# Performance work log

Measured on AMD Instinct MI355X. Metric: run time of the kernel, lower is better.

Reference implementation:

```python
import jax, jax.numpy as jnp
import numpy as np

SIZE = 5
DIM = 64


def setup_inputs() -> dict:
    key = jax.random.key(0)
    k0, k1, k2, k3, k4 = jax.random.split(key, 5)
    bs, C, H, W = 4, 3, 1024, 1024
    x = jax.random.uniform(k0, (bs, C, H, W), dtype=jnp.float32)
    n_off = SIZE * SIZE
    # conv1x1_{i}_E: Conv2d(1, DIM, 1) -> weight (DIM,1,1,1) ~= vector (DIM,), bias (DIM,)
    # conv1x1_{i}_S: Conv2d(DIM, 1, 1) -> weight (1,DIM,1,1) ~= vector (DIM,), bias ()
    wE = jax.random.normal(k1, (n_off, DIM), dtype=jnp.float32)            # fan_in=1 -> U(-1,1)-ish scale
    bE = jax.random.normal(k2, (n_off, DIM), dtype=jnp.float32) * 0.5
    wS = jax.random.normal(k3, (n_off, DIM), dtype=jnp.float32) * (1.0 / np.sqrt(DIM))
    bS = jax.random.normal(k4, (n_off,), dtype=jnp.float32) * 0.1
    return {"x": x, "wE": wE, "bE": bE, "wS": wS, "bS": bS}


def reference(x, wE, bE, wS, bS):
    size = SIZE
    pad = size // 2
    bs, C, H, W = x.shape
    xc = jnp.clip(x, 0.0, 1.0).reshape(bs * C, H, W)            # (N,H,W)
    xp = jnp.pad(xc, ((0, 0), (pad, pad), (pad, pad)), mode="reflect")
    # 25 shifted views, stacked: (K, N, H, W). Small fixed python loop over offsets.
    shifts = jnp.stack([xp[:, i:i + H, j:j + W]
                        for i in range(size) for j in range(size)])
    # Per offset k, S(E(x)) is linear in x (no nonlinearity between the 1x1 convs):
    #   out_k = (wS_k . wE_k) * x_k + (wS_k . bE_k + bS_k)
    a = jnp.einsum("kd,kd->k", wS, wE)                          # per-offset scale
    c = jnp.einsum("kd,kd->k", wS, bE) + bS                     # per-offset pixel-constant bias
    out = jnp.einsum("k,knhw->nhw", a, shifts) + c.sum()
    out = out / (size * size)
    out = jnp.clip(out, 0.0, 1.0)
    return out.reshape(bs, C, H, W)
```

## Files before the change

kernel.cpp:

```cpp
#include <hip/hip_runtime.h>
#include <hip/hip_bf16.h>


#define HH 1024
#define WW 1024
#define NIMG 12
#define TBH 8
#define ROWS (TBH + 4)
#define PF 6

typedef float f32x4 __attribute__((ext_vector_type(4)));
typedef float f32x2 __attribute__((ext_vector_type(2)));

__device__ __forceinline__ float readlane_f(float v, int lane) {
    return __int_as_float(__builtin_amdgcn_readlane(__float_as_int(v), lane));
}

__device__ __forceinline__ float sgpr_bcast(float v) {
    return __int_as_float(__builtin_amdgcn_readfirstlane(__float_as_int(v)));
}

__device__ __forceinline__ float dot4(f32x4 a, f32x4 b) {
    return a.x * b.x + a.y * b.y + a.z * b.z + a.w * b.w;
}

__device__ __forceinline__ f32x4 clip01v4(f32x4 v) {
    f32x4 z = {0.f, 0.f, 0.f, 0.f};
    f32x4 o = {1.f, 1.f, 1.f, 1.f};
    return __builtin_elementwise_min(__builtin_elementwise_max(v, z), o);
}

__device__ __forceinline__ f32x2 clip01v2(f32x2 v) {
    f32x2 z = {0.f, 0.f};
    f32x2 o = {1.f, 1.f};
    return __builtin_elementwise_min(__builtin_elementwise_max(v, z), o);
}

__global__ __launch_bounds__(256) void conv5_kernel(const float* __restrict__ x,
                                                    const float* __restrict__ wE,
                                                    const float* __restrict__ bE,
                                                    const float* __restrict__ wS,
                                                    const float* __restrict__ bS,
                                                    float* __restrict__ out) {
    int lane = threadIdx.x & 63;

    float apass[2], cacc = 0.f;
    #pragma unroll
    for (int p = 0; p < 2; ++p) {
        int k = p * 16 + (lane >> 2);
        float a = 0.f;
        if (k < 25) {
            int base = k * 64 + (lane & 3) * 16;
            #pragma unroll
            for (int i = 0; i < 4; ++i) {
                f32x4 sv = *(const f32x4*)(wS + base + 4 * i);
                f32x4 ev = *(const f32x4*)(wE + base + 4 * i);
                f32x4 bv = *(const f32x4*)(bE + base + 4 * i);
                a += dot4(sv, ev);
                cacc += dot4(sv, bv);
            }
        }
        a += __shfl_xor(a, 1);
        a += __shfl_xor(a, 2);
        apass[p] = a;
    }
    if (lane < 25) cacc += bS[lane];
    #pragma unroll
    for (int off = 32; off; off >>= 1) cacc += __shfl_xor(cacc, off);
    float bias = sgpr_bcast(cacc * (1.f / 25.f));
    f32x2 bias2 = {bias, bias};

    float wv[25];
    #pragma unroll
    for (int k = 0; k < 16; ++k) wv[k] = readlane_f(apass[0], 4 * k) * (1.f / 25.f);
    #pragma unroll
    for (int k = 16; k < 25; ++k) wv[k] = readlane_f(apass[1], 4 * (k - 16)) * (1.f / 25.f);

    int nwg = gridDim.x;
    int cpx = nwg >> 3;
    int l = (blockIdx.x & 7) * cpx + (blockIdx.x >> 3);
    int img = l >> 7;
    int rb = l & 127;
    int row0 = rb * TBH;

    const float* src = x + (size_t)img * (HH * WW);
    int tid = threadIdx.x;
    int cbase = tid * 4;

    bool lt = (cbase == 0);
    bool rt = (cbase == 1020);
    int qa = lt ? 0 : cbase - 2;
    int qb = rt ? 1020 : cbase + 2;

    auto rowptr = [&](int ir) -> const float* {
        int prow = row0 - 2 + ir;
        int sr = prow < 0 ? -prow : (prow >= HH ? 2 * HH - 2 - prow : prow);
        return src + (size_t)sr * WW;
    };

    f32x4 bufA[PF], bufB[PF];
    f32x2 acc[5][2];

    #pragma unroll
    for (int ir = 0; ir < PF; ++ir) {
        const float* rp = rowptr(ir);
        bufA[ir] = *(const f32x4*)(rp + qa);
        bufB[ir] = *(const f32x4*)(rp + qb);
    }
    __builtin_amdgcn_sched_barrier(0);

    float* op = out + (size_t)img * (HH * WW) + (size_t)row0 * WW + cbase;

    #pragma unroll
    for (int ir = 0; ir < ROWS; ++ir) {
        f32x4 A = bufA[ir % PF];
        f32x4 B = bufB[ir % PF];
        if (ir + PF < ROWS) {
            const float* rp = rowptr(ir + PF);
            bufA[ir % PF] = *(const f32x4*)(rp + qa);
            bufB[ir % PF] = *(const f32x4*)(rp + qb);
        }

        A = clip01v4(A);
        B = clip01v4(B);

        float r8[8] = {A.x, A.y, A.z, A.w, B.x, B.y, B.z, B.w};
        r8[0] = lt ? A.z : r8[0];
        r8[2] = lt ? A.x : r8[2];
        r8[3] = lt ? A.y : r8[3];
        r8[4] = rt ? B.z : r8[4];
        r8[5] = rt ? B.w : r8[5];
        r8[7] = rt ? B.y : r8[7];

        f32x2 pr[7];
        #pragma unroll
        for (int j = 0; j < 7; ++j) { pr[j].x = r8[j]; pr[j].y = r8[j + 1]; }

        if (ir < TBH) {
            acc[ir % 5][0] = bias2;
            acc[ir % 5][1] = bias2;
        }

        #pragma unroll
        for (int dr = 0; dr < 5; ++dr) {
            int orow = ir - dr;
            if (orow < 0 || orow >= TBH) continue;
            #pragma unroll
            for (int j = 0; j < 5; ++j) {
                float wj = wv[dr * 5 + j];
                f32x2 w2 = {wj, wj};
                acc[orow % 5][0] += pr[j] * w2;
                acc[orow % 5][1] += pr[j + 2] * w2;
            }
        }

        if (ir >= 4) {
            int orow = ir - 4;
            f32x2 lo = clip01v2(acc[orow % 5][0]);
            f32x2 hi = clip01v2(acc[orow % 5][1]);
            f32x4 o = {lo.x, lo.y, hi.x, hi.y};
            *(f32x4*)(op + (size_t)orow * WW) = o;
        }
    }
}

extern "C" void kernel_launch(void* const* d_in, const int* in_sizes, int n_in,
                              void* d_out, int out_size, void* d_ws, size_t ws_size,
                              hipStream_t stream) {
    const float* x  = (const float*)d_in[0];
    const float* wE = (const float*)d_in[1];
    const float* bE = (const float*)d_in[2];
    const float* wS = (const float*)d_in[3];
    const float* bS = (const float*)d_in[4];
    float* out = (float*)d_out;

    int nblocks = NIMG * (HH / TBH);
    conv5_kernel<<<nblocks, 256, 0, stream>>>(x, wE, bE, wS, bS, out);
}
```

Before: 25.67 us.

## Switch to persistent grid computing one output row per iteration

Replaces the 8-row register-blocked sliding window with a fixed grid of 2048 blocks, each looping over 6 single output rows strided across the whole tensor. Every output row now reloads its 5 input rows directly, so there is no vertical reuse in registers and each row is fetched about 5x instead of about 1.5x. The intent is to cut register pressure and per-block tail effects and to spread work evenly, relying on L2/MALL to absorb the redundant row loads. The risk is extra cache traffic and less in-flight prefetch depth.

```diff
diff --git a/kernel.cpp b/kernel.cpp
--- a/kernel.cpp
+++ b/kernel.cpp
@@ -5,9 +5,8 @@
 #define HH 1024
 #define WW 1024
 #define NIMG 12
-#define TBH 8
-#define ROWS (TBH + 4)
-#define PF 6
+#define NB 2048
+#define ITERS 6
 
 typedef float f32x4 __attribute__((ext_vector_type(4)));
 typedef float f32x2 __attribute__((ext_vector_type(2)));
@@ -15,21 +14,17 @@
 __device__ __forceinline__ float readlane_f(float v, int lane) {
     return __int_as_float(__builtin_amdgcn_readlane(__float_as_int(v), lane));
 }
-
 __device__ __forceinline__ float sgpr_bcast(float v) {
     return __int_as_float(__builtin_amdgcn_readfirstlane(__float_as_int(v)));
 }
-
 __device__ __forceinline__ float dot4(f32x4 a, f32x4 b) {
     return a.x * b.x + a.y * b.y + a.z * b.z + a.w * b.w;
 }
-
 __device__ __forceinline__ f32x4 clip01v4(f32x4 v) {
     f32x4 z = {0.f, 0.f, 0.f, 0.f};
     f32x4 o = {1.f, 1.f, 1.f, 1.f};
     return __builtin_elementwise_min(__builtin_elementwise_max(v, z), o);
 }
-
 __device__ __forceinline__ f32x2 clip01v2(f32x2 v) {
     f32x2 z = {0.f, 0.f};
     f32x2 o = {1.f, 1.f};
@@ -42,7 +37,8 @@
                                                     const float* __restrict__ wS,
                                                     const float* __restrict__ bS,
                                                     float* __restrict__ out) {
-    int lane = threadIdx.x & 63;
+    int tid  = threadIdx.x;
+    int lane = tid & 63;
 
     float apass[2], cacc = 0.f;
     #pragma unroll
@@ -76,91 +72,62 @@
     #pragma unroll
     for (int k = 16; k < 25; ++k) wv[k] = readlane_f(apass[1], 4 * (k - 16)) * (1.f / 25.f);
 
-    int nwg = gridDim.x;
-    int cpx = nwg >> 3;
-    int l = (blockIdx.x & 7) * cpx + (blockIdx.x >> 3);
-    int img = l >> 7;
-    int rb = l & 127;
-    int row0 = rb * TBH;
+    int l = (blockIdx.x & 7) * (NB >> 3) + (blockIdx.x >> 3);
 
-    const float* src = x + (size_t)img * (HH * WW);
-    int tid = threadIdx.x;
     int cbase = tid * 4;
-
     bool lt = (cbase == 0);
     bool rt = (cbase == 1020);
     int qa = lt ? 0 : cbase - 2;
     int qb = rt ? 1020 : cbase + 2;
 
-    auto rowptr = [&](int ir) -> const float* {
-        int prow = row0 - 2 + ir;
-        int sr = prow < 0 ? -prow : (prow >= HH ? 2 * HH - 2 - prow : prow);
-        return src + (size_t)sr * WW;
-    };
+    #pragma unroll 1
+    for (int it = 0; it < ITERS; ++it) {
+        int rid = l + it * NB;
+        int img = rid >> 10;
+        int row = rid & 1023;
+        const float* src = x + (size_t)img * (HH * WW);
 
-    f32x4 bufA[PF], bufB[PF];
-    f32x2 acc[5][2];
-
-    #pragma unroll
-    for (int ir = 0; ir < PF; ++ir) {
-        const float* rp = rowptr(ir);
-        bufA[ir] = *(const f32x4*)(rp + qa);
-        bufB[ir] = *(const f32x4*)(rp + qb);
-    }
-    __builtin_amdgcn_sched_barrier(0);
-
-    float* op = out + (size_t)img * (HH * WW) + (size_t)row0 * WW + cbase;
-
-    #pragma unroll
-    for (int ir = 0; ir < ROWS; ++ir) {
-        f32x4 A = bufA[ir % PF];
-        f32x4 B = bufB[ir % PF];
-        if (ir + PF < ROWS) {
-            const float* rp = rowptr(ir + PF);
-            bufA[ir % PF] = *(const f32x4*)(rp + qa);
-            bufB[ir % PF] = *(const f32x4*)(rp + qb);
+        f32x4 A[5], B[5];
+        #pragma unroll
+        for (int dr = 0; dr < 5; ++dr) {
+            int prow = row - 2 + dr;
+            int sr = prow < 0 ? -prow : (prow >= HH ? 2 * HH - 2 - prow : prow);
+            const float* rp = src + (size_t)sr * WW;
+            A[dr] = *(const f32x4*)(rp + qa);
+            B[dr] = *(const f32x4*)(rp + qb);
         }
 
-        A = clip01v4(A);
-        B = clip01v4(B);
-
-        float r8[8] = {A.x, A.y, A.z, A.w, B.x, B.y, B.z, B.w};
-        r8[0] = lt ? A.z : r8[0];
-        r8[2] = lt ? A.x : r8[2];
-        r8[3] = lt ? A.y : r8[3];
-        r8[4] = rt ? B.z : r8[4];
-        r8[5] = rt ? B.w : r8[5];
-        r8[7] = rt ? B.y : r8[7];
-
-        f32x2 pr[7];
-        #pragma unroll
-        for (int j = 0; j < 7; ++j) { pr[j].x = r8[j]; pr[j].y = r8[j + 1]; }
-
-        if (ir < TBH) {
-            acc[ir % 5][0] = bias2;
-            acc[ir % 5][1] = bias2;
-        }
-
+        f32x2 acc0 = bias2, acc1 = bias2;
         #pragma unroll
         for (int dr = 0; dr < 5; ++dr) {
-            int orow = ir - dr;
-            if (orow < 0 || orow >= TBH) continue;
+            f32x4 a = clip01v4(A[dr]);
+            f32x4 b = clip01v4(B[dr]);
+
+            float r8[8] = {a.x, a.y, a.z, a.w, b.x, b.y, b.z, b.w};
+            r8[0] = lt ? a.z : r8[0];
+            r8[2] = lt ? a.x : r8[2];
+            r8[3] = lt ? a.y : r8[3];
+            r8[4] = rt ? b.z : r8[4];
+            r8[5] = rt ? b.w : r8[5];
+            r8[7] = rt ? b.y : r8[7];
+
+            f32x2 pr[7];
+            #pragma unroll
+            for (int j = 0; j < 7; ++j) { pr[j].x = r8[j]; pr[j].y = r8[j + 1]; }
+
             #pragma unroll
             for (int j = 0; j < 5; ++j) {
                 float wj = wv[dr * 5 + j];
                 f32x2 w2 = {wj, wj};
-                acc[orow % 5][0] += pr[j] * w2;
-                acc[orow % 5][1] += pr[j + 2] * w2;
+                acc0 += pr[j] * w2;
+                acc1 += pr[j + 2] * w2;
             }
         }
 
-        if (ir >= 4) {
-            int orow = ir - 4;
-            f32x2 lo = clip01v2(acc[orow % 5][0]);
-            f32x2 hi = clip01v2(acc[orow % 5][1]);
-            f32x4 o = {lo.x, lo.y, hi.x, hi.y};
-            *(f32x4*)(op + (size_t)orow * WW) = o;
-        }
+        f32x2 lo = clip01v2(acc0);
+        f32x2 hi = clip01v2(acc1);
+        f32x4 o = {lo.x, lo.y, hi.x, hi.y};
+        *(f32x4*)(out + (size_t)img * (HH * WW) + (size_t)row * WW + cbase) = o;
     }
 }
 
@@ -174,6 +141,5 @@
     const float* bS = (const float*)d_in[4];
     float* out = (float*)d_out;
 
-    int nblocks = NIMG * (HH / TBH);
-    conv5_kernel<<<nblocks, 256, 0, stream>>>(x, wE, bE, wS, bS, out);
+    conv5_kernel<<<NB, 256, 0, stream>>>(x, wE, bE, wS, bS, out);
 }
```

After: 34.57 us. 1.35x slower.
